# Performance work log

Measured on AMD Instinct MI355X. Metric: run time of the kernel, lower is better.

The kernel has to match this reference:

```python
import jax, jax.numpy as jnp
import numpy as np

H = 1024
V = 50000
L = 2048


def setup_inputs() -> dict:
    key = jax.random.key(0)
    ks = jax.random.split(key, 16)
    s = 0.02  # weight init scale
    return {
        "input_tok": jax.random.randint(ks[0], (1,), 0, V, dtype=jnp.int64),
        "h0": jax.random.normal(ks[1], (1, 1, H), jnp.float32),
        "c0": jax.random.normal(ks[2], (1, 1, H), jnp.float32),
        "encoder_outputs": jax.random.normal(ks[3], (L, H), jnp.float32),
        "emb": jax.random.normal(ks[4], (V, H), jnp.float32) * s,
        "attn_W": jax.random.normal(ks[5], (H, H), jnp.float32) * s,
        "attn_b": jax.random.normal(ks[6], (H,), jnp.float32) * s,
        "comb_W": jax.random.normal(ks[7], (H, 2 * H), jnp.float32) * s,
        "comb_b": jax.random.normal(ks[8], (H,), jnp.float32) * s,
        "W_ih": jax.random.normal(ks[9], (4 * H, H), jnp.float32) * s,
        "W_hh": jax.random.normal(ks[10], (4 * H, H), jnp.float32) * s,
        "b_ih": jax.random.normal(ks[11], (4 * H,), jnp.float32) * s,
        "b_hh": jax.random.normal(ks[12], (4 * H,), jnp.float32) * s,
        "out_W": jax.random.normal(ks[13], (V, H), jnp.float32) * s,
        "out_b": jax.random.normal(ks[14], (V,), jnp.float32) * s,
    }


def reference(input_tok, h0, c0, encoder_outputs, emb, attn_W, attn_b,
              comb_W, comb_b, W_ih, W_hh, b_ih, b_hh, out_W, out_b):
    # embedded: [1, H] (single decode token; view(-1) in the source forces input_len == 1)
    e = emb[input_tok][0]  # [H]

    # attention branch (note: in the original module this result is dead code --
    # the loop below overwrites `output` -- but we compute it faithfully)
    scores = encoder_outputs @ (attn_W @ e + attn_b)        # [L]
    a = jax.nn.softmax(scores)                               # [L]
    ctx = a @ encoder_outputs                                # [H]
    combined = jnp.tanh(comb_W @ jnp.concatenate([e, ctx]) + comb_b)  # [H] (unused)

    # single LSTM cell step (torch gate order: i, f, g, o)
    h, c = h0[0, 0], c0[0, 0]                                # [H], [H]
    gates = W_ih @ e + b_ih + W_hh @ h + b_hh                # [4H]
    i, f, g, o = jnp.split(gates, 4)
    i, f, o = jax.nn.sigmoid(i), jax.nn.sigmoid(f), jax.nn.sigmoid(o)
    g = jnp.tanh(g)
    c_new = f * c + i * g
    h_new = o * jnp.tanh(c_new)

    # output projection + log_softmax over vocab
    logits = h_new @ out_W.T + out_b                         # [V]
    log_probs = jax.nn.log_softmax(logits)[None, :]          # [1, V]
    return log_probs, h_new[None, None, :], c_new[None, None, :]
```

## Files before the change

### kernel.cpp

```cpp
#include <hip/hip_runtime.h>
#include <math.h>

#define HH 1024
#define VV 50000

__device__ __forceinline__ float wredsum(float v) {
#pragma unroll
    for (int o = 32; o > 0; o >>= 1) v += __shfl_xor(v, o);
    return v;
}

__global__ __launch_bounds__(256) void lstm_kernel(
    const int* __restrict__ tok, const float* __restrict__ emb,
    const float* __restrict__ h0, const float* __restrict__ c0,
    const float* __restrict__ W_ih, const float* __restrict__ W_hh,
    const float* __restrict__ b_ih, const float* __restrict__ b_hh,
    float* __restrict__ out)
{
    const int wid  = threadIdx.x >> 6;
    const int lane = threadIdx.x & 63;
    const int j    = blockIdx.x * 4 + wid;
    const int t    = tok[0];
    const float* e = emb + (size_t)t * HH;

    float4 ev[4], hv[4];
#pragma unroll
    for (int k = 0; k < 4; ++k) {
        const int idx = k * 256 + lane * 4;
        ev[k] = *(const float4*)(e  + idx);
        hv[k] = *(const float4*)(h0 + idx);
    }

    float gate[4];
#pragma unroll
    for (int g = 0; g < 4; ++g) {
        const float* wi = W_ih + (size_t)(g * HH + j) * HH;
        const float* wh = W_hh + (size_t)(g * HH + j) * HH;
        float acc = 0.f;
#pragma unroll
        for (int k = 0; k < 4; ++k) {
            const int idx = k * 256 + lane * 4;
            const float4 a = *(const float4*)(wi + idx);
            const float4 b = *(const float4*)(wh + idx);
            acc += a.x * ev[k].x + a.y * ev[k].y + a.z * ev[k].z + a.w * ev[k].w;
            acc += b.x * hv[k].x + b.y * hv[k].y + b.z * hv[k].z + b.w * hv[k].w;
        }
        gate[g] = wredsum(acc);
    }

    if (lane == 0) {
        const float gi = gate[0] + b_ih[0 * HH + j] + b_hh[0 * HH + j];
        const float gf = gate[1] + b_ih[1 * HH + j] + b_hh[1 * HH + j];
        const float gg = gate[2] + b_ih[2 * HH + j] + b_hh[2 * HH + j];
        const float go = gate[3] + b_ih[3 * HH + j] + b_hh[3 * HH + j];
        const float si = 1.f / (1.f + expf(-gi));
        const float sf = 1.f / (1.f + expf(-gf));
        const float so = 1.f / (1.f + expf(-go));
        const float cn = sf * c0[j] + si * tanhf(gg);
        const float hn = so * tanhf(cn);
        out[VV + j]      = hn;
        out[VV + HH + j] = cn;
    }
}

__global__ __launch_bounds__(256) void logits_kernel(
    const float* __restrict__ out_W, const float* __restrict__ out_b,
    const float* __restrict__ h,
    float* __restrict__ logits,
    float* __restrict__ pmax, int nwaves)
{
    __shared__ float smax[4];
    const int wid  = threadIdx.x >> 6;
    const int lane = threadIdx.x & 63;
    const int gw   = blockIdx.x * 4 + wid;

    float4 hv[4];
#pragma unroll
    for (int k = 0; k < 4; ++k)
        hv[k] = *(const float4*)(h + k * 256 + lane * 4);

    float m = -INFINITY;
    for (int r = gw; r < VV; r += nwaves) {
        const float* w = out_W + (size_t)r * HH;
        float acc = 0.f;
#pragma unroll
        for (int k = 0; k < 4; ++k) {
            const float4 a = *(const float4*)(w + k * 256 + lane * 4);
            acc += a.x * hv[k].x + a.y * hv[k].y + a.z * hv[k].z + a.w * hv[k].w;
        }
        const float v = wredsum(acc) + out_b[r];
        if (lane == 0) logits[r] = v;
        m = fmaxf(m, v);
    }
    if (lane == 0) smax[wid] = m;
    __syncthreads();
    if (threadIdx.x == 0)
        pmax[blockIdx.x] = fmaxf(fmaxf(smax[0], smax[1]), fmaxf(smax[2], smax[3]));
}

__global__ __launch_bounds__(1024) void logz_kernel(
    const float* __restrict__ logits, const float* __restrict__ pmax,
    int nblk, float* __restrict__ logz)
{
    __shared__ float red[1024];
    float m = -INFINITY;
    for (int i = threadIdx.x; i < nblk; i += 1024) m = fmaxf(m, pmax[i]);
    red[threadIdx.x] = m;
    __syncthreads();
    for (int s = 512; s > 0; s >>= 1) {
        if (threadIdx.x < s)
            red[threadIdx.x] = fmaxf(red[threadIdx.x], red[threadIdx.x + s]);
        __syncthreads();
    }
    m = red[0];
    __syncthreads();

    float s = 0.f;
    for (int v = threadIdx.x; v < VV; v += 1024) s += expf(logits[v] - m);
    red[threadIdx.x] = s;
    __syncthreads();
    for (int st = 512; st > 0; st >>= 1) {
        if (threadIdx.x < st) red[threadIdx.x] += red[threadIdx.x + st];
        __syncthreads();
    }
    if (threadIdx.x == 0) *logz = m + logf(red[0]);
}

__global__ __launch_bounds__(256) void sub_kernel(
    float* __restrict__ logits, const float* __restrict__ logz)
{
    const float lz = *logz;
    const int v = blockIdx.x * 256 + threadIdx.x;
    if (v < VV) logits[v] -= lz;
}

extern "C" void kernel_launch(void* const* d_in, const int* in_sizes, int n_in,
                              void* d_out, int out_size, void* d_ws, size_t ws_size,
                              hipStream_t stream) {
    const int*   tok   = (const int*)  d_in[0];
    const float* h0    = (const float*)d_in[1];
    const float* c0    = (const float*)d_in[2];
    const float* emb   = (const float*)d_in[4];
    const float* W_ih  = (const float*)d_in[9];
    const float* W_hh  = (const float*)d_in[10];
    const float* b_ih  = (const float*)d_in[11];
    const float* b_hh  = (const float*)d_in[12];
    const float* out_W = (const float*)d_in[13];
    const float* out_b = (const float*)d_in[14];

    float* out = (float*)d_out;

    const int NB = 1250;
    float* pmax = (float*)d_ws;
    float* logz = pmax + NB;

    lstm_kernel<<<256, 256, 0, stream>>>(tok, emb, h0, c0, W_ih, W_hh, b_ih, b_hh, out);
    logits_kernel<<<NB, 256, 0, stream>>>(out_W, out_b, out + VV, out, pmax, NB * 4);
    logz_kernel<<<1, 1024, 0, stream>>>(out, pmax, NB, logz);
    sub_kernel<<<(VV + 255) / 256, 256, 0, stream>>>(out, logz);
}
```

Baseline: 431.5 us.

## Fuse online softmax partials into logits kernel and spread LSTM gates across blocks

Result: faster. 413.3 us (-4.2%).

```diff
diff --git a/kernel.cpp b/kernel.cpp
--- a/kernel.cpp
+++ b/kernel.cpp
@@ -3,6 +3,7 @@
 
 #define HH 1024
 #define VV 50000
+#define NB2 1250
 
 __device__ __forceinline__ float wredsum(float v) {
 #pragma unroll
@@ -17,46 +18,37 @@
     const float* __restrict__ b_ih, const float* __restrict__ b_hh,
     float* __restrict__ out)
 {
-    const int wid  = threadIdx.x >> 6;
+    __shared__ float sg[4];
+    const int g    = threadIdx.x >> 6;
     const int lane = threadIdx.x & 63;
-    const int j    = blockIdx.x * 4 + wid;
+    const int j    = blockIdx.x;
     const int t    = tok[0];
     const float* e = emb + (size_t)t * HH;
 
-    float4 ev[4], hv[4];
+    const float* wi = W_ih + (size_t)(g * HH + j) * HH;
+    const float* wh = W_hh + (size_t)(g * HH + j) * HH;
+
+    float acc = 0.f;
 #pragma unroll
     for (int k = 0; k < 4; ++k) {
         const int idx = k * 256 + lane * 4;
-        ev[k] = *(const float4*)(e  + idx);
-        hv[k] = *(const float4*)(h0 + idx);
+        const float4 a  = *(const float4*)(wi + idx);
+        const float4 b  = *(const float4*)(wh + idx);
+        const float4 ev = *(const float4*)(e  + idx);
+        const float4 hv = *(const float4*)(h0 + idx);
+        acc += a.x * ev.x + a.y * ev.y + a.z * ev.z + a.w * ev.w;
+        acc += b.x * hv.x + b.y * hv.y + b.z * hv.z + b.w * hv.w;
     }
+    acc = wredsum(acc);
+    if (lane == 0) sg[g] = acc + b_ih[g * HH + j] + b_hh[g * HH + j];
+    __syncthreads();
 
-    float gate[4];
-#pragma unroll
-    for (int g = 0; g < 4; ++g) {
-        const float* wi = W_ih + (size_t)(g * HH + j) * HH;
-        const float* wh = W_hh + (size_t)(g * HH + j) * HH;
-        float acc = 0.f;
-#pragma unroll
-        for (int k = 0; k < 4; ++k) {
-            const int idx = k * 256 + lane * 4;
-            const float4 a = *(const float4*)(wi + idx);
-            const float4 b = *(const float4*)(wh + idx);
-            acc += a.x * ev[k].x + a.y * ev[k].y + a.z * ev[k].z + a.w * ev[k].w;
-            acc += b.x * hv[k].x + b.y * hv[k].y + b.z * hv[k].z + b.w * hv[k].w;
-        }
-        gate[g] = wredsum(acc);
-    }
-
-    if (lane == 0) {
-        const float gi = gate[0] + b_ih[0 * HH + j] + b_hh[0 * HH + j];
-        const float gf = gate[1] + b_ih[1 * HH + j] + b_hh[1 * HH + j];
-        const float gg = gate[2] + b_ih[2 * HH + j] + b_hh[2 * HH + j];
-        const float go = gate[3] + b_ih[3 * HH + j] + b_hh[3 * HH + j];
-        const float si = 1.f / (1.f + expf(-gi));
-        const float sf = 1.f / (1.f + expf(-gf));
-        const float so = 1.f / (1.f + expf(-go));
-        const float cn = sf * c0[j] + si * tanhf(gg);
+    if (threadIdx.x == 0) {
+        const float si = 1.f / (1.f + expf(-sg[0]));
+        const float sf = 1.f / (1.f + expf(-sg[1]));
+        const float gg = tanhf(sg[2]);
+        const float so = 1.f / (1.f + expf(-sg[3]));
+        const float cn = sf * c0[j] + si * gg;
         const float hn = so * tanhf(cn);
         out[VV + j]      = hn;
         out[VV + HH + j] = cn;
@@ -67,9 +59,9 @@
     const float* __restrict__ out_W, const float* __restrict__ out_b,
     const float* __restrict__ h,
     float* __restrict__ logits,
-    float* __restrict__ pmax, int nwaves)
+    float2* __restrict__ part)
 {
-    __shared__ float smax[4];
+    __shared__ float2 sp[4];
     const int wid  = threadIdx.x >> 6;
     const int lane = threadIdx.x & 63;
     const int gw   = blockIdx.x * 4 + wid;
@@ -79,51 +71,68 @@
     for (int k = 0; k < 4; ++k)
         hv[k] = *(const float4*)(h + k * 256 + lane * 4);
 
-    float m = -INFINITY;
-    for (int r = gw; r < VV; r += nwaves) {
-        const float* w = out_W + (size_t)r * HH;
-        float acc = 0.f;
+    float m = -INFINITY, s = 0.f;
+#pragma unroll
+    for (int i = 0; i < 5; ++i) {
+        const int r0 = gw + (2 * i)     * 5000;
+        const int r1 = gw + (2 * i + 1) * 5000;
+        const float* w0 = out_W + (size_t)r0 * HH;
+        const float* w1 = out_W + (size_t)r1 * HH;
+        float a0 = 0.f, a1 = 0.f;
 #pragma unroll
         for (int k = 0; k < 4; ++k) {
-            const float4 a = *(const float4*)(w + k * 256 + lane * 4);
-            acc += a.x * hv[k].x + a.y * hv[k].y + a.z * hv[k].z + a.w * hv[k].w;
+            const int idx = k * 256 + lane * 4;
+            const float4 x0 = *(const float4*)(w0 + idx);
+            const float4 x1 = *(const float4*)(w1 + idx);
+            a0 += x0.x * hv[k].x + x0.y * hv[k].y + x0.z * hv[k].z + x0.w * hv[k].w;
+            a1 += x1.x * hv[k].x + x1.y * hv[k].y + x1.z * hv[k].z + x1.w * hv[k].w;
         }
-        const float v = wredsum(acc) + out_b[r];
-        if (lane == 0) logits[r] = v;
-        m = fmaxf(m, v);
+        const float v0 = wredsum(a0) + out_b[r0];
+        const float v1 = wredsum(a1) + out_b[r1];
+        if (lane == 0) { logits[r0] = v0; logits[r1] = v1; }
+        const float nm = fmaxf(m, fmaxf(v0, v1));
+        s = s * expf(m - nm) + expf(v0 - nm) + expf(v1 - nm);
+        m = nm;
     }
-    if (lane == 0) smax[wid] = m;
+    if (lane == 0) sp[wid] = make_float2(m, s);
     __syncthreads();
-    if (threadIdx.x == 0)
-        pmax[blockIdx.x] = fmaxf(fmaxf(smax[0], smax[1]), fmaxf(smax[2], smax[3]));
+    if (threadIdx.x == 0) {
+        float2 p = sp[0];
+#pragma unroll
+        for (int w = 1; w < 4; ++w) {
+            const float2 q = sp[w];
+            const float nm = fmaxf(p.x, q.x);
+            p.y = p.y * expf(p.x - nm) + q.y * expf(q.x - nm);
+            p.x = nm;
+        }
+        part[blockIdx.x] = p;
+    }
 }
 
-__global__ __launch_bounds__(1024) void logz_kernel(
-    const float* __restrict__ logits, const float* __restrict__ pmax,
-    int nblk, float* __restrict__ logz)
+__global__ __launch_bounds__(256) void logz_kernel(
+    const float2* __restrict__ part, int nblk, float* __restrict__ logz)
 {
-    __shared__ float red[1024];
-    float m = -INFINITY;
-    for (int i = threadIdx.x; i < nblk; i += 1024) m = fmaxf(m, pmax[i]);
-    red[threadIdx.x] = m;
+    __shared__ float2 red[256];
+    float m = -INFINITY, s = 0.f;
+    for (int i = threadIdx.x; i < nblk; i += 256) {
+        const float2 q = part[i];
+        const float nm = fmaxf(m, q.x);
+        s = s * expf(m - nm) + q.y * expf(q.x - nm);
+        m = nm;
+    }
+    red[threadIdx.x] = make_float2(m, s);
     __syncthreads();
-    for (int s = 512; s > 0; s >>= 1) {
-        if (threadIdx.x < s)
-            red[threadIdx.x] = fmaxf(red[threadIdx.x], red[threadIdx.x + s]);
+    for (int st = 128; st > 0; st >>= 1) {
+        if (threadIdx.x < st) {
+            float2 p = red[threadIdx.x], q = red[threadIdx.x + st];
+            const float nm = fmaxf(p.x, q.x);
+            p.y = p.y * expf(p.x - nm) + q.y * expf(q.x - nm);
+            p.x = nm;
+            red[threadIdx.x] = p;
+        }
         __syncthreads();
     }
-    m = red[0];
-    __syncthreads();
-
-    float s = 0.f;
-    for (int v = threadIdx.x; v < VV; v += 1024) s += expf(logits[v] - m);
-    red[threadIdx.x] = s;
-    __syncthreads();
-    for (int st = 512; st > 0; st >>= 1) {
-        if (threadIdx.x < st) red[threadIdx.x] += red[threadIdx.x + st];
-        __syncthreads();
-    }
-    if (threadIdx.x == 0) *logz = m + logf(red[0]);
+    if (threadIdx.x == 0) *logz = red[0].x + logf(red[0].y);
 }
 
 __global__ __launch_bounds__(256) void sub_kernel(
@@ -150,12 +159,11 @@
 
     float* out = (float*)d_out;
 
-    const int NB = 1250;
-    float* pmax = (float*)d_ws;
-    float* logz = pmax + NB;
+    float2* part = (float2*)d_ws;
+    float*  logz = (float*)(part + NB2);
 
-    lstm_kernel<<<256, 256, 0, stream>>>(tok, emb, h0, c0, W_ih, W_hh, b_ih, b_hh, out);
-    logits_kernel<<<NB, 256, 0, stream>>>(out_W, out_b, out + VV, out, pmax, NB * 4);
-    logz_kernel<<<1, 1024, 0, stream>>>(out, pmax, NB, logz);
+    lstm_kernel<<<1024, 256, 0, stream>>>(tok, emb, h0, c0, W_ih, W_hh, b_ih, b_hh, out);
+    logits_kernel<<<NB2, 256, 0, stream>>>(out_W, out_b, out + VV, out, part);
+    logz_kernel<<<1, 256, 0, stream>>>(part, NB2, logz);
     sub_kernel<<<(VV + 255) / 256, 256, 0, stream>>>(out, logz);
 }
```
